# Performance work log

Measured on AMD Instinct MI355X. Metric: run time of the kernel, lower is better.

The kernel has to match this reference:

```python
import jax, jax.numpy as jnp
import numpy as np

B, L, E, H = 2, 2048, 1024, 16
D = E // H  # head dim = 64


def setup_inputs() -> dict:
    key = jax.random.key(0)
    ks = jax.random.split(key, 10)
    s = 0.02
    return {
        "xt": jax.random.normal(ks[0], (B, L, E), jnp.float32),
        "xs": jax.random.normal(ks[1], (B, L, E), jnp.float32),
        "Wt": jax.random.normal(ks[2], (E, 3 * E), jnp.float32) * s,  # t_attn weight (x @ Wt)
        "bt": jnp.zeros((3 * E,), jnp.float32),
        "Ws": jax.random.normal(ks[3], (E, 2 * E), jnp.float32) * s,  # s_attn weight
        "bs": jnp.zeros((2 * E,), jnp.float32),
        "Wc": jax.random.normal(ks[4], (E, E), jnp.float32) * s,      # c_proj weight
        "bc": jnp.zeros((E,), jnp.float32),
        "lam_ts": jnp.ones((1,), jnp.float32),
        "lam_st": jnp.ones((1,), jnp.float32),
        "lam_ss": jnp.ones((1,), jnp.float32),
    }


def _heads(x):
    # (B, L, E) -> (B, H, L, D)
    return x.reshape(B, L, H, D).transpose(0, 2, 1, 3)


def reference(xt, xs, Wt, bt, Ws, bs, Wc, bc, lam_ts, lam_st, lam_ss):
    qt, kt, vt = jnp.split(xt @ Wt + bt, 3, axis=2)
    qs, ks = jnp.split(xs @ Ws + bs, 2, axis=2)
    qt, kt, vt, qs, ks = map(_heads, (qt, kt, vt, qs, ks))

    # 4-way disentangled scores; fuse the 4 matmuls into 2 by combining keys:
    # qt@kt^T + lam_ts*qt@ks^T = qt @ (kt + lam_ts*ks)^T
    # lam_st*qs@kt^T + lam_ss*qs@ks^T = qs @ (lam_st*kt + lam_ss*ks)^T
    k1 = kt + lam_ts[0] * ks
    k2 = lam_st[0] * kt + lam_ss[0] * ks
    att = (jnp.einsum('bhqd,bhkd->bhqk', qt, k1)
           + jnp.einsum('bhqd,bhkd->bhqk', qs, k2)) * (1.0 / np.sqrt(D))
    att = jax.nn.softmax(att, axis=-1)
    y = jnp.einsum('bhqk,bhkd->bhqd', att, vt)  # (B, H, L, D)
    y = y.transpose(0, 2, 1, 3).reshape(B, L, E)
    return y @ Wc + bc
```

## Files before the change

### kernel.cpp

```cpp
#include <hip/hip_runtime.h>
#include <math.h>

#define LQ 2048
#define EQ 1024
#define M_ROWS 4096
#define BH 32

typedef _Float16 f16x8 __attribute__((ext_vector_type(8)));
typedef _Float16 f16x4 __attribute__((ext_vector_type(4)));
typedef float f32x4 __attribute__((ext_vector_type(4)));

#define QSCALE 0.1803368801111204f

__device__ __forceinline__ void async_ld16(const _Float16* g, _Float16* l) {
  __builtin_amdgcn_global_load_lds(
      (const __attribute__((address_space(1))) unsigned int*)g,
      (__attribute__((address_space(3))) unsigned int*)l, 16, 0, 0);
}

__global__ __launch_bounds__(256) void convert_x(
    const float* __restrict__ xt, const float* __restrict__ xs,
    _Float16* __restrict__ xt16, _Float16* __restrict__ xs16) {
  int i = blockIdx.x * 256 + threadIdx.x;
  const float* s; _Float16* d; size_t off;
  if (i < 524288) { s = xt; d = xt16; off = (size_t)i * 8; }
  else            { s = xs; d = xs16; off = (size_t)(i - 524288) * 8; }
  float4 a = *(const float4*)&s[off];
  float4 b = *(const float4*)&s[off + 4];
  f16x8 h;
  h[0] = (_Float16)a.x; h[1] = (_Float16)a.y; h[2] = (_Float16)a.z; h[3] = (_Float16)a.w;
  h[4] = (_Float16)b.x; h[5] = (_Float16)b.y; h[6] = (_Float16)b.z; h[7] = (_Float16)b.w;
  *(f16x8*)&d[off] = h;
}

__global__ __launch_bounds__(256) void transpose_w(
    const float* __restrict__ Wt, const float* __restrict__ Ws,
    const float* __restrict__ Wc,
    _Float16* __restrict__ WtT, _Float16* __restrict__ WsT,
    _Float16* __restrict__ WcT) {
  __shared__ float T[32][33];
  int tx = threadIdx.x & 31, ty = threadIdx.x >> 5;
  int c0 = blockIdx.x * 32;
  int k0 = blockIdx.y * 32;
  const float* W; _Float16* D; int Nw, cl;
  if (c0 < 3072)      { W = Wt; D = WtT; Nw = 3072; cl = c0; }
  else if (c0 < 5120) { W = Ws; D = WsT; Nw = 2048; cl = c0 - 3072; }
  else                { W = Wc; D = WcT; Nw = 1024; cl = c0 - 5120; }
#pragma unroll
  for (int j = 0; j < 4; ++j)
    T[ty + j * 8][tx] = W[(size_t)(k0 + ty + j * 8) * Nw + cl + tx];
  __syncthreads();
#pragma unroll
  for (int j = 0; j < 4; ++j)
    D[(size_t)(cl + ty + j * 8) * 1024 + k0 + tx] = (_Float16)T[tx][ty + j * 8];
}

__global__ __launch_bounds__(256) void gemm_bt(
    const _Float16* __restrict__ A, const _Float16* __restrict__ Bm,
    const float* __restrict__ bias,
    float* __restrict__ outf, _Float16* __restrict__ q16,
    _Float16* __restrict__ k16, _Float16* __restrict__ v16,
    int N, int mode) {
  __shared__ _Float16 Al[128 * 32];
  __shared__ _Float16 Bl[128 * 32];

  const int tid = threadIdx.x;
  const int w = tid >> 6;
  const int lane = tid & 63;
  const int quad = lane >> 4;
  const int l15 = lane & 15;
  const int wm = w >> 1, wn = w & 1;
  const int m0 = blockIdx.y * 128;
  const int n0 = blockIdx.x * 128;

  const int srow = lane >> 2;
  const int schunk = ((lane & 3) ^ ((lane >> 3) & 3)) * 8;

  f32x4 acc[4][4];
#pragma unroll
  for (int mb = 0; mb < 4; ++mb)
#pragma unroll
    for (int nb = 0; nb < 4; ++nb) acc[mb][nb] = (f32x4){0.f, 0.f, 0.f, 0.f};

  const int key = (l15 >> 1) & 3;

  for (int kt = 0; kt < 1024; kt += 32) {
    __syncthreads();
#pragma unroll
    for (int i = 0; i < 2; ++i) {
      int rt = w * 32 + i * 16;
      async_ld16(&A[(size_t)(m0 + rt + srow) * 1024 + kt + schunk], &Al[rt * 32]);
      async_ld16(&Bm[(size_t)(n0 + rt + srow) * 1024 + kt + schunk], &Bl[rt * 32]);
    }
    __syncthreads();

    f16x8 af[4], bf[4];
    const int pc = (quad ^ key) * 8;
#pragma unroll
    for (int mb = 0; mb < 4; ++mb)
      af[mb] = *(f16x8*)&Al[(wm * 64 + mb * 16 + l15) * 32 + pc];
#pragma unroll
    for (int nb = 0; nb < 4; ++nb)
      bf[nb] = *(f16x8*)&Bl[(wn * 64 + nb * 16 + l15) * 32 + pc];
#pragma unroll
    for (int mb = 0; mb < 4; ++mb)
#pragma unroll
      for (int nb = 0; nb < 4; ++nb)
        acc[mb][nb] = __builtin_amdgcn_mfma_f32_16x16x32_f16(af[mb], bf[nb], acc[mb][nb], 0, 0, 0);
  }

#pragma unroll
  for (int mb = 0; mb < 4; ++mb)
#pragma unroll
    for (int nb = 0; nb < 4; ++nb)
#pragma unroll
      for (int r = 0; r < 4; ++r) {
        int row = m0 + wm * 64 + mb * 16 + quad * 4 + r;
        int col = n0 + wn * 64 + nb * 16 + l15;
        float val = acc[mb][nb][r] + bias[col];
        if (mode == 2) {
          outf[(size_t)row * 1024 + col] = val;
        } else {
          int bb = row >> 11, ll = row & 2047;
          int which = col >> 10, e = col & 1023;
          int hh = e >> 6, dd = e & 63;
          size_t rowhd = (size_t)(bb * 16 + hh) * 2048 + ll;
          if (mode == 0) {
            if (which == 0)      q16[rowhd * 128 + dd] = (_Float16)(val * QSCALE);
            else if (which == 1) k16[rowhd * 128 + dd] = (_Float16)val;
            else                 v16[rowhd * 64 + dd] = (_Float16)val;
          } else {
            if (which == 0) q16[rowhd * 128 + 64 + dd] = (_Float16)(val * QSCALE);
            else            k16[rowhd * 128 + 64 + dd] = (_Float16)val;
          }
        }
      }
}

__global__ __launch_bounds__(256) void combine16(
    _Float16* __restrict__ kcat, const float* __restrict__ lam_ts,
    const float* __restrict__ lam_st, const float* __restrict__ lam_ss) {
  int idx = blockIdx.x * 256 + threadIdx.x;
  int row = idx >> 3;
  int d8 = (idx & 7) * 8;
  float lts = lam_ts[0], lst = lam_st[0], lss = lam_ss[0];
  size_t base = (size_t)row * 128;
  f16x8 a = *(f16x8*)&kcat[base + d8];
  f16x8 b = *(f16x8*)&kcat[base + 64 + d8];
  f16x8 o1, o2;
#pragma unroll
  for (int e = 0; e < 8; ++e) {
    float kt = (float)a[e], ks = (float)b[e];
    o1[e] = (_Float16)(kt + lts * ks);
    o2[e] = (_Float16)(lst * kt + lss * ks);
  }
  *(f16x8*)&kcat[base + d8] = o1;
  *(f16x8*)&kcat[base + 64 + d8] = o2;
}

__global__ __launch_bounds__(512, 4) void flash_attn_mfma(
    const _Float16* __restrict__ qcat, const _Float16* __restrict__ kcat,
    const _Float16* __restrict__ v, _Float16* __restrict__ y) {
  const int bh = blockIdx.y;
  const int qt0 = blockIdx.x * 128;
  const int b = bh >> 4, h = bh & 15;
  const _Float16* Qg = qcat + (size_t)bh * LQ * 128;
  const _Float16* Kg = kcat + (size_t)bh * LQ * 128;
  const _Float16* Vg = v + (size_t)bh * LQ * 64;

  __shared__ _Float16 Ksh[64 * 128];
  __shared__ _Float16 Vt[64 * 72];
  __shared__ _Float16 Psh[8 * 16 * 72];

  const int tid = threadIdx.x;
  const int w = tid >> 6;
  const int lane = tid & 63;
  const int quad = lane >> 4;
  const int l15 = lane & 15;

  f16x8 qf[4];
#pragma unroll
  for (int db = 0; db < 4; ++db)
    qf[db] = *(const f16x8*)&Qg[(size_t)(qt0 + w * 16 + l15) * 128 + db * 32 + quad * 8];

  float m_i = -INFINITY;
  float l_i = 0.f;
  f32x4 O[4];
#pragma unroll
  for (int nb = 0; nb < 4; ++nb) O[nb] = (f32x4){0.f, 0.f, 0.f, 0.f};

  _Float16* Pw = &Psh[w * 16 * 72];

  int krow[2], kgc[2];
#pragma unroll
  for (int a = 0; a < 2; ++a) {
    krow[a] = w * 8 + a * 4 + (lane >> 4);
    kgc[a] = (lane & 15) ^ (krow[a] & 7);
  }
  const _Float16* vsrc = Vg + (size_t)lane * 64 + w * 8;
  f16x8 vv = *(const f16x8*)vsrc;

  for (int t = 0; t < LQ; t += 64) {
    __syncthreads();

#pragma unroll
    for (int a = 0; a < 2; ++a)
      async_ld16(&Kg[(size_t)(t + krow[a]) * 128 + kgc[a] * 8],
                 &Ksh[(w * 8 + a * 4) * 128]);

#pragma unroll
    for (int e = 0; e < 8; ++e) Vt[(w * 8 + e) * 72 + lane] = vv[e];
    if (t + 64 < LQ) vv = *(const f16x8*)(vsrc + (size_t)(t + 64) * 64);

    __syncthreads();

    f32x4 S[4];
#pragma unroll
    for (int kb = 0; kb < 4; ++kb) S[kb] = (f32x4){0.f, 0.f, 0.f, 0.f};
#pragma unroll
    for (int db = 0; db < 4; ++db) {
      const int pc = ((db * 4 + quad) ^ (l15 & 7)) * 8;
      f16x8 af[4];
#pragma unroll
      for (int kb = 0; kb < 4; ++kb)
        af[kb] = *(f16x8*)&Ksh[(kb * 16 + l15) * 128 + pc];
#pragma unroll
      for (int kb = 0; kb < 4; ++kb)
        S[kb] = __builtin_amdgcn_mfma_f32_16x16x32_f16(af[kb], qf[db], S[kb], 0, 0, 0);
    }

    float mx = -INFINITY;
#pragma unroll
    for (int kb = 0; kb < 4; ++kb)
#pragma unroll
      for (int r = 0; r < 4; ++r) mx = fmaxf(mx, S[kb][r]);
    mx = fmaxf(mx, __shfl_xor(mx, 16));
    mx = fmaxf(mx, __shfl_xor(mx, 32));
    float m_new = fmaxf(m_i, mx);
    float alpha = __builtin_amdgcn_exp2f(m_i - m_new);
    float s = 0.f;
#pragma unroll
    for (int kb = 0; kb < 4; ++kb)
#pragma unroll
      for (int r = 0; r < 4; ++r) {
        float p = __builtin_amdgcn_exp2f(S[kb][r] - m_new);
        S[kb][r] = p;
        s += p;
      }
    s += __shfl_xor(s, 16);
    s += __shfl_xor(s, 32);
    l_i = l_i * alpha + s;
    m_i = m_new;

#pragma unroll
    for (int kb = 0; kb < 4; ++kb) {
      f16x4 p4;
      p4[0] = (_Float16)S[kb][0];
      p4[1] = (_Float16)S[kb][1];
      p4[2] = (_Float16)S[kb][2];
      p4[3] = (_Float16)S[kb][3];
      *(f16x4*)&Pw[l15 * 72 + kb * 16 + quad * 4] = p4;
    }

#pragma unroll
    for (int r = 0; r < 4; ++r) {
      float ab = __shfl(alpha, quad * 4 + r);
#pragma unroll
      for (int nb = 0; nb < 4; ++nb) O[nb][r] *= ab;
    }

#pragma unroll
    for (int kb2 = 0; kb2 < 2; ++kb2) {
      f16x8 ap = *(f16x8*)&Pw[l15 * 72 + kb2 * 32 + quad * 8];
      f16x8 bv[4];
#pragma unroll
      for (int nb = 0; nb < 4; ++nb)
        bv[nb] = *(f16x8*)&Vt[(nb * 16 + l15) * 72 + kb2 * 32 + quad * 8];
#pragma unroll
      for (int nb = 0; nb < 4; ++nb)
        O[nb] = __builtin_amdgcn_mfma_f32_16x16x32_f16(ap, bv[nb], O[nb], 0, 0, 0);
    }
  }

#pragma unroll
  for (int r = 0; r < 4; ++r) {
    float li = __shfl(l_i, quad * 4 + r);
    float inv = 1.f / li;
    int qrow = qt0 + w * 16 + quad * 4 + r;
#pragma unroll
    for (int nb = 0; nb < 4; ++nb)
      y[((size_t)b * LQ + qrow) * EQ + h * 64 + nb * 16 + l15] = (_Float16)(O[nb][r] * inv);
  }
}

extern "C" void kernel_launch(void* const* d_in, const int* in_sizes, int n_in,
                              void* d_out, int out_size, void* d_ws, size_t ws_size,
                              hipStream_t stream) {
  const float* xt = (const float*)d_in[0];
  const float* xs = (const float*)d_in[1];
  const float* Wt = (const float*)d_in[2];
  const float* bt = (const float*)d_in[3];
  const float* Ws = (const float*)d_in[4];
  const float* bs = (const float*)d_in[5];
  const float* Wc = (const float*)d_in[6];
  const float* bc = (const float*)d_in[7];
  const float* lam_ts = (const float*)d_in[8];
  const float* lam_st = (const float*)d_in[9];
  const float* lam_ss = (const float*)d_in[10];
  float* out = (float*)d_out;

  _Float16* w16 = (_Float16*)d_ws;
  _Float16* xt16 = w16;
  _Float16* xs16 = xt16 + 4194304;
  _Float16* WtT  = xs16 + 4194304;
  _Float16* WsT  = WtT + 3145728;
  _Float16* WcT  = WsT + 2097152;
  _Float16* qcat = WcT + 1048576;
  _Float16* kcat = qcat + 8388608;
  _Float16* vbuf = kcat + 8388608;
  _Float16* ybuf = vbuf + 4194304;

  convert_x<<<4096, 256, 0, stream>>>(xt, xs, xt16, xs16);
  transpose_w<<<dim3(192, 32), 256, 0, stream>>>(Wt, Ws, Wc, WtT, WsT, WcT);
  gemm_bt<<<dim3(24, 32), 256, 0, stream>>>(
      xt16, WtT, bt, nullptr, qcat, kcat, vbuf, 3072, 0);
  gemm_bt<<<dim3(16, 32), 256, 0, stream>>>(
      xs16, WsT, bs, nullptr, qcat, kcat, nullptr, 2048, 1);
  combine16<<<2048, 256, 0, stream>>>(kcat, lam_ts, lam_st, lam_ss);
  flash_attn_mfma<<<dim3(16, 32), 512, 0, stream>>>(qcat, kcat, vbuf, ybuf);
  gemm_bt<<<dim3(8, 32), 256, 0, stream>>>(
      ybuf, WcT, bc, out, nullptr, nullptr, nullptr, 1024, 2);
}
```

Before: 304.7 us.

## Use 32x32 MFMA in flash attention, fuse key combine into GEMM, transpose V

The flash attention kernel is rebuilt around 32x32x16 MFMA tiles. Each of 4 waves (256 threads) now owns 32 query rows, which drops the cross-lane shuffles used for alpha and l. The V projection is written transposed by the QKV GEMM epilogue, so V can be loaded into LDS asynchronously with a swizzle instead of through a register transpose. The separate combine16 kernel is removed and the lambda key combination is folded into the xs GEMM epilogue, which reads the kt values back. That readback makes the epilogue depend on the earlier GEMM having finished, and the transposed V stores are strided, uncoalesced writes.

```diff
diff --git a/kernel.cpp b/kernel.cpp
--- a/kernel.cpp
+++ b/kernel.cpp
@@ -9,6 +9,7 @@
 typedef _Float16 f16x8 __attribute__((ext_vector_type(8)));
 typedef _Float16 f16x4 __attribute__((ext_vector_type(4)));
 typedef float f32x4 __attribute__((ext_vector_type(4)));
+typedef float f32x16 __attribute__((ext_vector_type(16)));
 
 #define QSCALE 0.1803368801111204f
 
@@ -60,6 +61,8 @@
     const float* __restrict__ bias,
     float* __restrict__ outf, _Float16* __restrict__ q16,
     _Float16* __restrict__ k16, _Float16* __restrict__ v16,
+    const float* __restrict__ lam_ts, const float* __restrict__ lam_st,
+    const float* __restrict__ lam_ss,
     int N, int mode) {
   __shared__ _Float16 Al[128 * 32];
   __shared__ _Float16 Bl[128 * 32];
@@ -75,6 +78,9 @@
 
   const int srow = lane >> 2;
   const int schunk = ((lane & 3) ^ ((lane >> 3) & 3)) * 8;
+
+  float lts = 0.f, lst = 0.f, lss = 0.f;
+  if (mode == 1) { lts = lam_ts[0]; lst = lam_st[0]; lss = lam_ss[0]; }
 
   f32x4 acc[4][4];
 #pragma unroll
@@ -128,169 +134,154 @@
           if (mode == 0) {
             if (which == 0)      q16[rowhd * 128 + dd] = (_Float16)(val * QSCALE);
             else if (which == 1) k16[rowhd * 128 + dd] = (_Float16)val;
-            else                 v16[rowhd * 64 + dd] = (_Float16)val;
+            else                 v16[((size_t)(bb * 16 + hh) * 64 + dd) * 2048 + ll] = (_Float16)val;
           } else {
-            if (which == 0) q16[rowhd * 128 + 64 + dd] = (_Float16)(val * QSCALE);
-            else            k16[rowhd * 128 + 64 + dd] = (_Float16)val;
+            if (which == 0) {
+              q16[rowhd * 128 + 64 + dd] = (_Float16)(val * QSCALE);
+            } else {
+              float ktv = (float)k16[rowhd * 128 + dd];
+              float ksv = val;
+              k16[rowhd * 128 + dd]      = (_Float16)(ktv + lts * ksv);
+              k16[rowhd * 128 + 64 + dd] = (_Float16)(lst * ktv + lss * ksv);
+            }
           }
         }
       }
 }
 
-__global__ __launch_bounds__(256) void combine16(
-    _Float16* __restrict__ kcat, const float* __restrict__ lam_ts,
-    const float* __restrict__ lam_st, const float* __restrict__ lam_ss) {
-  int idx = blockIdx.x * 256 + threadIdx.x;
-  int row = idx >> 3;
-  int d8 = (idx & 7) * 8;
-  float lts = lam_ts[0], lst = lam_st[0], lss = lam_ss[0];
-  size_t base = (size_t)row * 128;
-  f16x8 a = *(f16x8*)&kcat[base + d8];
-  f16x8 b = *(f16x8*)&kcat[base + 64 + d8];
-  f16x8 o1, o2;
-#pragma unroll
-  for (int e = 0; e < 8; ++e) {
-    float kt = (float)a[e], ks = (float)b[e];
-    o1[e] = (_Float16)(kt + lts * ks);
-    o2[e] = (_Float16)(lst * kt + lss * ks);
-  }
-  *(f16x8*)&kcat[base + d8] = o1;
-  *(f16x8*)&kcat[base + 64 + d8] = o2;
-}
-
-__global__ __launch_bounds__(512, 4) void flash_attn_mfma(
+__global__ __launch_bounds__(256, 2) void flash_attn_mfma(
     const _Float16* __restrict__ qcat, const _Float16* __restrict__ kcat,
-    const _Float16* __restrict__ v, _Float16* __restrict__ y) {
+    const _Float16* __restrict__ vT, _Float16* __restrict__ y) {
   const int bh = blockIdx.y;
   const int qt0 = blockIdx.x * 128;
   const int b = bh >> 4, h = bh & 15;
   const _Float16* Qg = qcat + (size_t)bh * LQ * 128;
   const _Float16* Kg = kcat + (size_t)bh * LQ * 128;
-  const _Float16* Vg = v + (size_t)bh * LQ * 64;
+  const _Float16* Vg = vT + (size_t)bh * 64 * LQ;
 
   __shared__ _Float16 Ksh[64 * 128];
-  __shared__ _Float16 Vt[64 * 72];
-  __shared__ _Float16 Psh[8 * 16 * 72];
+  __shared__ _Float16 Vsh[64 * 64];
+  __shared__ _Float16 Psh[4 * 32 * 72];
 
   const int tid = threadIdx.x;
   const int w = tid >> 6;
   const int lane = tid & 63;
-  const int quad = lane >> 4;
-  const int l15 = lane & 15;
-
-  f16x8 qf[4];
-#pragma unroll
-  for (int db = 0; db < 4; ++db)
-    qf[db] = *(const f16x8*)&Qg[(size_t)(qt0 + w * 16 + l15) * 128 + db * 32 + quad * 8];
+  const int half = lane >> 5;
+  const int l31 = lane & 31;
+
+  f16x8 qf[8];
+#pragma unroll
+  for (int db = 0; db < 8; ++db)
+    qf[db] = *(const f16x8*)&Qg[(size_t)(qt0 + w * 32 + l31) * 128 + db * 16 + half * 8];
 
   float m_i = -INFINITY;
   float l_i = 0.f;
-  f32x4 O[4];
-#pragma unroll
-  for (int nb = 0; nb < 4; ++nb) O[nb] = (f32x4){0.f, 0.f, 0.f, 0.f};
-
-  _Float16* Pw = &Psh[w * 16 * 72];
-
-  int krow[2], kgc[2];
-#pragma unroll
-  for (int a = 0; a < 2; ++a) {
-    krow[a] = w * 8 + a * 4 + (lane >> 4);
-    kgc[a] = (lane & 15) ^ (krow[a] & 7);
-  }
-  const _Float16* vsrc = Vg + (size_t)lane * 64 + w * 8;
-  f16x8 vv = *(const f16x8*)vsrc;
+  f32x16 O[2];
+#pragma unroll
+  for (int nt = 0; nt < 2; ++nt)
+#pragma unroll
+    for (int r = 0; r < 16; ++r) O[nt][r] = 0.f;
+
+  _Float16* Pw = &Psh[w * 32 * 72];
 
   for (int t = 0; t < LQ; t += 64) {
     __syncthreads();
 
 #pragma unroll
-    for (int a = 0; a < 2; ++a)
-      async_ld16(&Kg[(size_t)(t + krow[a]) * 128 + kgc[a] * 8],
-                 &Ksh[(w * 8 + a * 4) * 128]);
-
-#pragma unroll
-    for (int e = 0; e < 8; ++e) Vt[(w * 8 + e) * 72 + lane] = vv[e];
-    if (t + 64 < LQ) vv = *(const f16x8*)(vsrc + (size_t)(t + 64) * 64);
-
+    for (int a = 0; a < 4; ++a) {
+      int row = w * 16 + a * 4 + (lane >> 4);
+      int sc = (lane & 15) ^ (row & 7);
+      async_ld16(&Kg[(size_t)(t + row) * 128 + sc * 8], &Ksh[(w * 16 + a * 4) * 128]);
+    }
+#pragma unroll
+    for (int a = 0; a < 2; ++a) {
+      int row = w * 16 + a * 8 + (lane >> 3);
+      int sc = (lane & 7) ^ (row & 7);
+      async_ld16(&Vg[(size_t)row * LQ + t + sc * 8], &Vsh[(w * 16 + a * 8) * 64]);
+    }
     __syncthreads();
 
-    f32x4 S[4];
-#pragma unroll
-    for (int kb = 0; kb < 4; ++kb) S[kb] = (f32x4){0.f, 0.f, 0.f, 0.f};
-#pragma unroll
-    for (int db = 0; db < 4; ++db) {
-      const int pc = ((db * 4 + quad) ^ (l15 & 7)) * 8;
-      f16x8 af[4];
-#pragma unroll
-      for (int kb = 0; kb < 4; ++kb)
-        af[kb] = *(f16x8*)&Ksh[(kb * 16 + l15) * 128 + pc];
-#pragma unroll
-      for (int kb = 0; kb < 4; ++kb)
-        S[kb] = __builtin_amdgcn_mfma_f32_16x16x32_f16(af[kb], qf[db], S[kb], 0, 0, 0);
+    f32x16 S[2];
+#pragma unroll
+    for (int kb = 0; kb < 2; ++kb)
+#pragma unroll
+      for (int r = 0; r < 16; ++r) S[kb][r] = 0.f;
+#pragma unroll
+    for (int db = 0; db < 8; ++db) {
+      const int pc = ((db * 2 + half) ^ (lane & 7)) * 8;
+      f16x8 af[2];
+#pragma unroll
+      for (int kb = 0; kb < 2; ++kb)
+        af[kb] = *(f16x8*)&Ksh[(kb * 32 + l31) * 128 + pc];
+#pragma unroll
+      for (int kb = 0; kb < 2; ++kb)
+        S[kb] = __builtin_amdgcn_mfma_f32_32x32x16_f16(af[kb], qf[db], S[kb], 0, 0, 0);
     }
 
     float mx = -INFINITY;
 #pragma unroll
-    for (int kb = 0; kb < 4; ++kb)
-#pragma unroll
-      for (int r = 0; r < 4; ++r) mx = fmaxf(mx, S[kb][r]);
-    mx = fmaxf(mx, __shfl_xor(mx, 16));
+    for (int kb = 0; kb < 2; ++kb)
+#pragma unroll
+      for (int r = 0; r < 16; ++r) mx = fmaxf(mx, S[kb][r]);
     mx = fmaxf(mx, __shfl_xor(mx, 32));
     float m_new = fmaxf(m_i, mx);
     float alpha = __builtin_amdgcn_exp2f(m_i - m_new);
     float s = 0.f;
 #pragma unroll
-    for (int kb = 0; kb < 4; ++kb)
-#pragma unroll
-      for (int r = 0; r < 4; ++r) {
+    for (int kb = 0; kb < 2; ++kb)
+#pragma unroll
+      for (int r = 0; r < 16; ++r) {
         float p = __builtin_amdgcn_exp2f(S[kb][r] - m_new);
         S[kb][r] = p;
         s += p;
       }
-    s += __shfl_xor(s, 16);
     s += __shfl_xor(s, 32);
     l_i = l_i * alpha + s;
     m_i = m_new;
 
 #pragma unroll
+    for (int kb = 0; kb < 2; ++kb)
+#pragma unroll
+      for (int rg = 0; rg < 4; ++rg) {
+        f16x4 p4;
+#pragma unroll
+        for (int i = 0; i < 4; ++i) p4[i] = (_Float16)S[kb][rg * 4 + i];
+        *(f16x4*)&Pw[l31 * 72 + kb * 32 + rg * 8 + half * 4] = p4;
+      }
+
+#pragma unroll
+    for (int nt = 0; nt < 2; ++nt)
+#pragma unroll
+      for (int r = 0; r < 16; ++r) O[nt][r] *= alpha;
+
+#pragma unroll
     for (int kb = 0; kb < 4; ++kb) {
-      f16x4 p4;
-      p4[0] = (_Float16)S[kb][0];
-      p4[1] = (_Float16)S[kb][1];
-      p4[2] = (_Float16)S[kb][2];
-      p4[3] = (_Float16)S[kb][3];
-      *(f16x4*)&Pw[l15 * 72 + kb * 16 + quad * 4] = p4;
-    }
-
-#pragma unroll
-    for (int r = 0; r < 4; ++r) {
-      float ab = __shfl(alpha, quad * 4 + r);
-#pragma unroll
-      for (int nb = 0; nb < 4; ++nb) O[nb][r] *= ab;
-    }
-
-#pragma unroll
-    for (int kb2 = 0; kb2 < 2; ++kb2) {
-      f16x8 ap = *(f16x8*)&Pw[l15 * 72 + kb2 * 32 + quad * 8];
-      f16x8 bv[4];
-#pragma unroll
-      for (int nb = 0; nb < 4; ++nb)
-        bv[nb] = *(f16x8*)&Vt[(nb * 16 + l15) * 72 + kb2 * 32 + quad * 8];
-#pragma unroll
-      for (int nb = 0; nb < 4; ++nb)
-        O[nb] = __builtin_amdgcn_mfma_f32_16x16x32_f16(ap, bv[nb], O[nb], 0, 0, 0);
+      f16x8 pb = *(f16x8*)&Pw[l31 * 72 + kb * 16 + half * 8];
+      f16x8 av[2];
+#pragma unroll
+      for (int nt = 0; nt < 2; ++nt) {
+        int dim = nt * 32 + l31;
+        int pc = ((kb * 2 + half) ^ (dim & 7)) * 8;
+        av[nt] = *(f16x8*)&Vsh[dim * 64 + pc];
+      }
+#pragma unroll
+      for (int nt = 0; nt < 2; ++nt)
+        O[nt] = __builtin_amdgcn_mfma_f32_32x32x16_f16(av[nt], pb, O[nt], 0, 0, 0);
     }
   }
 
-#pragma unroll
-  for (int r = 0; r < 4; ++r) {
-    float li = __shfl(l_i, quad * 4 + r);
-    float inv = 1.f / li;
-    int qrow = qt0 + w * 16 + quad * 4 + r;
-#pragma unroll
-    for (int nb = 0; nb < 4; ++nb)
-      y[((size_t)b * LQ + qrow) * EQ + h * 64 + nb * 16 + l15] = (_Float16)(O[nb][r] * inv);
-  }
+  float inv = 1.f / l_i;
+  int qrow = qt0 + w * 32 + l31;
+#pragma unroll
+  for (int nt = 0; nt < 2; ++nt)
+#pragma unroll
+    for (int rg = 0; rg < 4; ++rg) {
+      f16x4 o4;
+#pragma unroll
+      for (int i = 0; i < 4; ++i) o4[i] = (_Float16)(O[nt][rg * 4 + i] * inv);
+      int dim = nt * 32 + rg * 8 + half * 4;
+      *(f16x4*)&y[((size_t)b * LQ + qrow) * EQ + h * 64 + dim] = o4;
+    }
 }
 
 extern "C" void kernel_launch(void* const* d_in, const int* in_sizes, int n_in,
@@ -317,17 +308,16 @@
   _Float16* WcT  = WsT + 2097152;
   _Float16* qcat = WcT + 1048576;
   _Float16* kcat = qcat + 8388608;
-  _Float16* vbuf = kcat + 8388608;
-  _Float16* ybuf = vbuf + 4194304;
+  _Float16* vbufT = kcat + 8388608;
+  _Float16* ybuf = vbufT + 4194304;
 
   convert_x<<<4096, 256, 0, stream>>>(xt, xs, xt16, xs16);
   transpose_w<<<dim3(192, 32), 256, 0, stream>>>(Wt, Ws, Wc, WtT, WsT, WcT);
   gemm_bt<<<dim3(24, 32), 256, 0, stream>>>(
-      xt16, WtT, bt, nullptr, qcat, kcat, vbuf, 3072, 0);
+      xt16, WtT, bt, nullptr, qcat, kcat, vbufT, nullptr, nullptr, nullptr, 3072, 0);
   gemm_bt<<<dim3(16, 32), 256, 0, stream>>>(
-      xs16, WsT, bs, nullptr, qcat, kcat, nullptr, 2048, 1);
-  combine16<<<2048, 256, 0, stream>>>(kcat, lam_ts, lam_st, lam_ss);
-  flash_attn_mfma<<<dim3(16, 32), 512, 0, stream>>>(qcat, kcat, vbuf, ybuf);
+      xs16, WsT, bs, nullptr, qcat, kcat, nullptr, lam_ts, lam_st, lam_ss, 2048, 1);
+  flash_attn_mfma<<<dim3(16, 32), 256, 0, stream>>>(qcat, kcat, vbufT, ybuf);
   gemm_bt<<<dim3(8, 32), 256, 0, stream>>>(
-      ybuf, WcT, bc, out, nullptr, nullptr, nullptr, 1024, 2);
-}
+      ybuf, WcT, bc, out, nullptr, nullptr, nullptr, nullptr, nullptr, nullptr, 1024, 2);
+}
```

Measured after the change: 292.7 us. 3.9% less time.
